# Kernel tuning notes

Measured on AMD Instinct MI355X. Metric: run time of the kernel, lower is better.

The kernel has to match this reference:

```python
import jax, jax.numpy as jnp
import numpy as np

DIM = 1024
NUM_HEADS = 16
HEAD_DIM = DIM // NUM_HEADS


def setup_inputs() -> dict:
    key = jax.random.key(0)
    k1, k2, k3, k4, k5 = jax.random.split(key, 5)
    B, N = 4, 2048
    x = jax.random.normal(k1, (B, N, DIM), dtype=jnp.float32)
    s_in = 1.0 / np.sqrt(DIM)
    W_qkv = jax.random.normal(k2, (DIM, 3 * DIM), dtype=jnp.float32) * s_in
    b_qkv = jax.random.normal(k3, (3 * DIM,), dtype=jnp.float32) * 0.02
    W_proj = jax.random.normal(k4, (DIM, DIM), dtype=jnp.float32) * s_in
    b_proj = jax.random.normal(k5, (DIM,), dtype=jnp.float32) * 0.02
    return {"x": x, "W_qkv": W_qkv, "b_qkv": b_qkv, "W_proj": W_proj, "b_proj": b_proj}


def reference(x, W_qkv, b_qkv, W_proj, b_proj):
    B, N, C = x.shape
    H, D = NUM_HEADS, HEAD_DIM
    scale = D ** -0.5
    qkv = x @ W_qkv + b_qkv                      # [B, N, 3C]
    qkv = qkv.reshape(B, N, 3, H, D)
    q = jnp.transpose(qkv[:, :, 0], (0, 2, 1, 3))  # [B, H, N, D]
    k = jnp.transpose(qkv[:, :, 1], (0, 2, 1, 3))
    v = jnp.transpose(qkv[:, :, 2], (0, 2, 1, 3))
    # scaled dot-product attention (dropout_p=0 in eval)
    attn = jnp.einsum("bhqd,bhkd->bhqk", q, k) * scale
    attn = jax.nn.softmax(attn, axis=-1)
    o = jnp.einsum("bhqk,bhkd->bhqd", attn, v)   # [B, H, N, D]
    o = jnp.transpose(o, (0, 2, 1, 3)).reshape(B, N, C)
    return o @ W_proj + b_proj
```

## Files before the change

### kernel.cpp

```cpp
#include <hip/hip_runtime.h>
#include <cstdint>

#define DIMC 1024
#define NHEAD 16
#define HD 64
#define SEQ 2048
#define NTOK 8192

typedef __attribute__((ext_vector_type(8))) short bfrag;
typedef __attribute__((ext_vector_type(4))) short spack4;
typedef __attribute__((ext_vector_type(4))) float fv4;
typedef __attribute__((ext_vector_type(16))) float f32x16;
typedef __attribute__((ext_vector_type(4))) int iv4;

static __device__ __forceinline__ unsigned short f2bf(float f) {
  union { float f; unsigned int u; } v; v.f = f;
  return (unsigned short)((v.u + 0x7fffu + ((v.u >> 16) & 1u)) >> 16);
}
static __device__ __forceinline__ unsigned int pack2(float a, float b) {
  return (unsigned int)f2bf(a) | ((unsigned int)f2bf(b) << 16);
}

#define MFMA(a, b, c) __builtin_amdgcn_mfma_f32_16x16x32_bf16((a), (b), (c), 0, 0, 0)
#define MFMA32(a, b, c) __builtin_amdgcn_mfma_f32_32x32x16_bf16((a), (b), (c), 0, 0, 0)

__global__ void cvt_x(const float* __restrict__ x, short* __restrict__ xb) {
  int i = (blockIdx.x * 256 + threadIdx.x) * 4;
  fv4 v = *(const fv4*)&x[i];
  spack4 o;
#pragma unroll
  for (int j = 0; j < 4; ++j) o[j] = (short)f2bf(v[j]);
  *(spack4*)&xb[i] = o;
}

__global__ void transpose_w(const float* __restrict__ W, short* __restrict__ WT,
                            int R, int C) {
  __shared__ float tile[32][33];
  const int t = threadIdx.x;
  const int r = t >> 3, c4 = t & 7;
  const int r0 = blockIdx.y * 32, c0 = blockIdx.x * 32;
  fv4 v = *(const fv4*)&W[(size_t)(r0 + r) * C + c0 + c4 * 4];
#pragma unroll
  for (int j = 0; j < 4; ++j) tile[r][c4 * 4 + j] = v[j];
  __syncthreads();
  spack4 o;
#pragma unroll
  for (int j = 0; j < 4; ++j) o[j] = (short)f2bf(tile[c4 * 4 + j][r]);
  *(spack4*)&WT[(size_t)(c0 + r) * R + r0 + c4 * 4] = o;
}

template <int MODE>
__launch_bounds__(256)
__global__ void gemm_bt(const short* __restrict__ A, const short* __restrict__ BT,
                        const float* __restrict__ bias, int M, int N, int K,
                        short* __restrict__ out0, short* __restrict__ out1,
                        short* __restrict__ out2, float* __restrict__ outf) {
  __shared__ alignas(16) char As[128 * 128];
  __shared__ alignas(16) char Bs[128 * 128];
  const int t = threadIdx.x;
  const int lane = t & 63;
  const int wid = t >> 6;
  const int wm = wid >> 1, wn = wid & 1;
  const int g = lane >> 4, l15 = lane & 15;
  const int row0 = blockIdx.y * 128;
  const int col0 = blockIdx.x * 128;
  const int lr = t >> 3, ls = t & 7;

  fv4 acc[4][4] = {};

  for (int k0 = 0; k0 < K; k0 += 64) {
    bfrag av[4], bv[4];
#pragma unroll
    for (int i = 0; i < 4; ++i) {
      int row = lr + i * 32;
      av[i] = *(const bfrag*)&A[(size_t)(row0 + row) * K + k0 + ls * 8];
      bv[i] = *(const bfrag*)&BT[(size_t)(col0 + row) * K + k0 + ls * 8];
    }
    __syncthreads();
#pragma unroll
    for (int i = 0; i < 4; ++i) {
      int row = lr + i * 32;
      int kb = (ls * 16) ^ ((row & 7) << 4);
      *(bfrag*)&As[row * 128 + kb] = av[i];
      *(bfrag*)&Bs[row * 128 + kb] = bv[i];
    }
    __syncthreads();
#pragma unroll
    for (int kk = 0; kk < 2; ++kk) {
      bfrag af[4], bf[4];
#pragma unroll
      for (int mm = 0; mm < 4; ++mm) {
        int row = wm * 64 + mm * 16 + l15;
        af[mm] = *(const bfrag*)&As[row * 128 + ((kk * 64 + g * 16) ^ ((row & 7) << 4))];
      }
#pragma unroll
      for (int nn = 0; nn < 4; ++nn) {
        int row = wn * 64 + nn * 16 + l15;
        bf[nn] = *(const bfrag*)&Bs[row * 128 + ((kk * 64 + g * 16) ^ ((row & 7) << 4))];
      }
#pragma unroll
      for (int mm = 0; mm < 4; ++mm)
#pragma unroll
        for (int nn = 0; nn < 4; ++nn)
          acc[mm][nn] = MFMA(af[mm], bf[nn], acc[mm][nn]);
    }
  }

  if (MODE == 0) {
    const float qs = 0.125f * 1.4426950408889634f;
#pragma unroll
    for (int nn = 0; nn < 4; ++nn) {
      int col = col0 + wn * 64 + nn * 16 + l15;
      int which = col >> 10;
      int rem = col & 1023;
      int h = rem >> 6, d = rem & 63;
      float bval = bias[col];
#pragma unroll
      for (int mm = 0; mm < 4; ++mm) {
        int tok = row0 + wm * 64 + mm * 16 + g * 4;
        int b = tok >> 11, n = tok & 2047;
        int bh = b * NHEAD + h;
        if (which == 0) {
#pragma unroll
          for (int r = 0; r < 4; ++r)
            out0[((size_t)bh * SEQ + n + r) * HD + d] =
                (short)f2bf((acc[mm][nn][r] + bval) * qs);
        } else if (which == 1) {
#pragma unroll
          for (int r = 0; r < 4; ++r)
            out1[((size_t)bh * SEQ + n + r) * HD + d] =
                (short)f2bf(acc[mm][nn][r] + bval);
        } else {
          spack4 p;
#pragma unroll
          for (int r = 0; r < 4; ++r) p[r] = (short)f2bf(acc[mm][nn][r] + bval);
          *(spack4*)&out2[((size_t)bh * HD + d) * SEQ + n] = p;
        }
      }
    }
  } else {
#pragma unroll
    for (int nn = 0; nn < 4; ++nn) {
      int col = col0 + wn * 64 + nn * 16 + l15;
      float bval = bias[col];
#pragma unroll
      for (int mm = 0; mm < 4; ++mm) {
        int tok = row0 + wm * 64 + mm * 16 + g * 4;
#pragma unroll
        for (int r = 0; r < 4; ++r)
          outf[(size_t)(tok + r) * N + col] = acc[mm][nn][r] + bval;
      }
    }
  }
}

__launch_bounds__(256, 3)
__global__ void attn_fwd(const short* __restrict__ Q, const short* __restrict__ Kb,
                         const short* __restrict__ VT, short* __restrict__ O) {
  __shared__ alignas(16) char Ks[2][8192];
  __shared__ alignas(16) char Vs[2][8192];

  const int t = threadIdx.x, lane = t & 63, wid = t >> 6;
  const int l31 = lane & 31, hi = lane >> 5, l7 = lane & 7;

  const int bid = blockIdx.x;
  const int xcd = bid & 7, mm_ = bid >> 3;
  const int bh = xcd + 8 * (mm_ >> 4);
  const int qt = mm_ & 15;

  const size_t base = (size_t)bh * SEQ * HD;
  const short* Qp = Q + base;
  const short* Kp = Kb + base;
  const short* Vp = VT + base;
  const int q0 = qt * 128 + wid * 32;

  bfrag qf[4];
#pragma unroll
  for (int dblk = 0; dblk < 4; ++dblk)
    qf[dblk] = *(const bfrag*)&Qp[(size_t)(q0 + l31) * HD + dblk * 16 + hi * 8];

  f32x16 oacc[2] = {};
  float m = -1e30f, l = 0.f;

  const int sr = t >> 3, ss = t & 7;
  const int swz0 = (ss * 16) ^ ((sr & 7) << 4);

  {
    bfrag k0 = *(const bfrag*)&Kp[(size_t)sr * HD + ss * 8];
    bfrag k1 = *(const bfrag*)&Kp[(size_t)(32 + sr) * HD + ss * 8];
    bfrag v0 = *(const bfrag*)&Vp[(size_t)sr * SEQ + ss * 8];
    bfrag v1 = *(const bfrag*)&Vp[(size_t)(sr + 32) * SEQ + ss * 8];
    *(bfrag*)&Ks[0][sr * 128 + swz0] = k0;
    *(bfrag*)&Ks[0][(sr + 32) * 128 + swz0] = k1;
    *(bfrag*)&Vs[0][sr * 128 + swz0] = v0;
    *(bfrag*)&Vs[0][(sr + 32) * 128 + swz0] = v1;
  }
  __syncthreads();

  int cur = 0;
  for (int kt = 0; kt < SEQ / 64; ++kt) {
    bfrag nk0, nk1, nv0, nv1;
    const bool pre = (kt + 1) < (SEQ / 64);
    if (pre) {
      const int kb2 = (kt + 1) * 64;
      nk0 = *(const bfrag*)&Kp[(size_t)(kb2 + sr) * HD + ss * 8];
      nk1 = *(const bfrag*)&Kp[(size_t)(kb2 + 32 + sr) * HD + ss * 8];
      nv0 = *(const bfrag*)&Vp[(size_t)sr * SEQ + kb2 + ss * 8];
      nv1 = *(const bfrag*)&Vp[(size_t)(sr + 32) * SEQ + kb2 + ss * 8];
    }

    const char* Kc = Ks[cur];
    const char* Vc = Vs[cur];

    f32x16 sf[2] = {};
#pragma unroll
    for (int kb = 0; kb < 2; ++kb) {
#pragma unroll
      for (int dblk = 0; dblk < 4; ++dblk) {
        const int row = kb * 32 + l31;
        bfrag kf = *(const bfrag*)&Kc[row * 128 + ((dblk * 32 + hi * 16) ^ (l7 << 4))];
        sf[kb] = MFMA32(kf, qf[dblk], sf[kb]);
      }
    }

    float pm = sf[0][0];
#pragma unroll
    for (int i = 1; i < 16; ++i) pm = fmaxf(pm, sf[0][i]);
#pragma unroll
    for (int i = 0; i < 16; ++i) pm = fmaxf(pm, sf[1][i]);
    pm = fmaxf(pm, __shfl_xor(pm, 32));

    {
      const float mn = fmaxf(m, pm);
      const float corr = __builtin_amdgcn_exp2f(m - mn);
      m = mn;
      l *= corr;
#pragma unroll
      for (int dh = 0; dh < 2; ++dh)
#pragma unroll
        for (int i = 0; i < 16; ++i) oacc[dh][i] *= corr;
    }

    float sum = 0.f;
#pragma unroll
    for (int kb = 0; kb < 2; ++kb)
#pragma unroll
      for (int i = 0; i < 16; ++i) {
        const float e = __builtin_amdgcn_exp2f(sf[kb][i] - m);
        sf[kb][i] = e;
        sum += e;
      }
    l += sum + __shfl_xor(sum, 32);

#pragma unroll
    for (int hb = 0; hb < 4; ++hb) {
      const int kb = hb >> 1, ob = (hb & 1) * 8;
      const unsigned int x01 = pack2(sf[kb][ob + 0], sf[kb][ob + 1]);
      const unsigned int x23 = pack2(sf[kb][ob + 2], sf[kb][ob + 3]);
      const unsigned int y45 = pack2(sf[kb][ob + 4], sf[kb][ob + 5]);
      const unsigned int y67 = pack2(sf[kb][ob + 6], sf[kb][ob + 7]);
      const unsigned int px01 = (unsigned int)__shfl_xor((int)x01, 32);
      const unsigned int px23 = (unsigned int)__shfl_xor((int)x23, 32);
      const unsigned int py45 = (unsigned int)__shfl_xor((int)y45, 32);
      const unsigned int py67 = (unsigned int)__shfl_xor((int)y67, 32);
      iv4 pw;
      pw[0] = (int)(hi ? py45 : x01);
      pw[1] = (int)(hi ? py67 : x23);
      pw[2] = (int)(hi ? y45 : px01);
      pw[3] = (int)(hi ? y67 : px23);
      const bfrag pb = __builtin_bit_cast(bfrag, pw);
#pragma unroll
      for (int dh = 0; dh < 2; ++dh) {
        const int row = dh * 32 + l31;
        bfrag vf = *(const bfrag*)&Vc[row * 128 + ((hb * 32 + hi * 16) ^ (l7 << 4))];
        oacc[dh] = MFMA32(vf, pb, oacc[dh]);
      }
    }

    if (pre) {
      const int nb = cur ^ 1;
      *(bfrag*)&Ks[nb][sr * 128 + swz0] = nk0;
      *(bfrag*)&Ks[nb][(sr + 32) * 128 + swz0] = nk1;
      *(bfrag*)&Vs[nb][sr * 128 + swz0] = nv0;
      *(bfrag*)&Vs[nb][(sr + 32) * 128 + swz0] = nv1;
      __syncthreads();
    }
    cur ^= 1;
  }

  const float inv = 1.0f / l;
  const int b = bh >> 4, h = bh & 15;
  const int q = q0 + l31;
#pragma unroll
  for (int dh = 0; dh < 2; ++dh)
#pragma unroll
    for (int gp = 0; gp < 4; ++gp) {
      const int d0 = dh * 32 + gp * 8 + hi * 4;
      spack4 pk;
#pragma unroll
      for (int j = 0; j < 4; ++j)
        pk[j] = (short)f2bf(oacc[dh][gp * 4 + j] * inv);
      *(spack4*)&O[((size_t)b * SEQ + q) * DIMC + h * HD + d0] = pk;
    }
}

extern "C" void kernel_launch(void* const* d_in, const int* in_sizes, int n_in,
                              void* d_out, int out_size, void* d_ws, size_t ws_size,
                              hipStream_t stream) {
  const float* x     = (const float*)d_in[0];
  const float* Wqkv  = (const float*)d_in[1];
  const float* bqkv  = (const float*)d_in[2];
  const float* Wproj = (const float*)d_in[3];
  const float* bproj = (const float*)d_in[4];
  float* out = (float*)d_out;
  char* ws = (char*)d_ws;

  short* xb  = (short*)(ws);
  short* WqT = (short*)(ws + 16777216);
  short* WpT = (short*)(ws + 23068672);
  short* Qb  = (short*)(ws + 25165824);
  short* Kb  = (short*)(ws + 41943040);
  short* VTb = (short*)(ws + 58720256);
  short* Ob  = (short*)(ws + 75497472);

  cvt_x<<<8192, 256, 0, stream>>>(x, xb);
  transpose_w<<<dim3(96, 32), 256, 0, stream>>>(Wqkv, WqT, 1024, 3072);
  transpose_w<<<dim3(32, 32), 256, 0, stream>>>(Wproj, WpT, 1024, 1024);
  gemm_bt<0><<<dim3(24, 64), 256, 0, stream>>>(xb, WqT, bqkv, NTOK, 3072, 1024,
                                               Qb, Kb, VTb, nullptr);
  attn_fwd<<<1024, 256, 0, stream>>>(Qb, Kb, VTb, Ob);
  gemm_bt<1><<<dim3(8, 64), 256, 0, stream>>>(Ob, WpT, bproj, NTOK, 1024, 1024,
                                              nullptr, nullptr, nullptr, out);
}
```

Baseline: 228.8 us.

## Use direct global-to-LDS loads in GEMM and drop P-fragment lane shuffles in attention

```diff
diff --git a/kernel.cpp b/kernel.cpp
--- a/kernel.cpp
+++ b/kernel.cpp
@@ -1,4 +1,5 @@
 #include <hip/hip_runtime.h>
+#include <hip/hip_bf16.h>
 #include <cstdint>
 
 #define DIMC 1024
@@ -17,12 +18,21 @@
   union { float f; unsigned int u; } v; v.f = f;
   return (unsigned short)((v.u + 0x7fffu + ((v.u >> 16) & 1u)) >> 16);
 }
-static __device__ __forceinline__ unsigned int pack2(float a, float b) {
-  return (unsigned int)f2bf(a) | ((unsigned int)f2bf(b) << 16);
+static __device__ __forceinline__ unsigned int pack2c(float a, float b) {
+  __hip_bfloat16 ha(a), hb(b);
+  unsigned short ua, ub;
+  __builtin_memcpy(&ua, &ha, 2);
+  __builtin_memcpy(&ub, &hb, 2);
+  return (unsigned int)ua | ((unsigned int)ub << 16);
 }
 
 #define MFMA(a, b, c) __builtin_amdgcn_mfma_f32_16x16x32_bf16((a), (b), (c), 0, 0, 0)
 #define MFMA32(a, b, c) __builtin_amdgcn_mfma_f32_32x32x16_bf16((a), (b), (c), 0, 0, 0)
+
+#define GLOAD_LDS(gp, lp)                                                  \
+  __builtin_amdgcn_global_load_lds(                                        \
+      (const __attribute__((address_space(1))) void*)(gp),                 \
+      (__attribute__((address_space(3))) void*)(lp), 16, 0, 0)
 
 __global__ void cvt_x(const float* __restrict__ x, short* __restrict__ xb) {
   int i = (blockIdx.x * 256 + threadIdx.x) * 4;
@@ -64,25 +74,17 @@
   const int g = lane >> 4, l15 = lane & 15;
   const int row0 = blockIdx.y * 128;
   const int col0 = blockIdx.x * 128;
-  const int lr = t >> 3, ls = t & 7;
 
   fv4 acc[4][4] = {};
 
+  const int srow = t >> 3, sk = (t & 7) * 8;
+
   for (int k0 = 0; k0 < K; k0 += 64) {
-    bfrag av[4], bv[4];
 #pragma unroll
     for (int i = 0; i < 4; ++i) {
-      int row = lr + i * 32;
-      av[i] = *(const bfrag*)&A[(size_t)(row0 + row) * K + k0 + ls * 8];
-      bv[i] = *(const bfrag*)&BT[(size_t)(col0 + row) * K + k0 + ls * 8];
-    }
-    __syncthreads();
-#pragma unroll
-    for (int i = 0; i < 4; ++i) {
-      int row = lr + i * 32;
-      int kb = (ls * 16) ^ ((row & 7) << 4);
-      *(bfrag*)&As[row * 128 + kb] = av[i];
-      *(bfrag*)&Bs[row * 128 + kb] = bv[i];
+      const int row = i * 32 + srow;
+      GLOAD_LDS(&A[(size_t)(row0 + row) * K + k0 + sk], &As[i * 4096 + t * 16]);
+      GLOAD_LDS(&BT[(size_t)(col0 + row) * K + k0 + sk], &Bs[i * 4096 + t * 16]);
     }
     __syncthreads();
 #pragma unroll
@@ -91,12 +93,12 @@
 #pragma unroll
       for (int mm = 0; mm < 4; ++mm) {
         int row = wm * 64 + mm * 16 + l15;
-        af[mm] = *(const bfrag*)&As[row * 128 + ((kk * 64 + g * 16) ^ ((row & 7) << 4))];
+        af[mm] = *(const bfrag*)&As[row * 128 + kk * 64 + g * 16];
       }
 #pragma unroll
       for (int nn = 0; nn < 4; ++nn) {
         int row = wn * 64 + nn * 16 + l15;
-        bf[nn] = *(const bfrag*)&Bs[row * 128 + ((kk * 64 + g * 16) ^ ((row & 7) << 4))];
+        bf[nn] = *(const bfrag*)&Bs[row * 128 + kk * 64 + g * 16];
       }
 #pragma unroll
       for (int mm = 0; mm < 4; ++mm)
@@ -104,6 +106,7 @@
         for (int nn = 0; nn < 4; ++nn)
           acc[mm][nn] = MFMA(af[mm], bf[nn], acc[mm][nn]);
     }
+    __syncthreads();
   }
 
   if (MODE == 0) {
@@ -131,10 +134,11 @@
             out1[((size_t)bh * SEQ + n + r) * HD + d] =
                 (short)f2bf(acc[mm][nn][r] + bval);
         } else {
+          int n2 = (n & ~15) | ((n & 4) << 1) | ((n & 8) >> 1);
           spack4 p;
 #pragma unroll
           for (int r = 0; r < 4; ++r) p[r] = (short)f2bf(acc[mm][nn][r] + bval);
-          *(spack4*)&out2[((size_t)bh * HD + d) * SEQ + n] = p;
+          *(spack4*)&out2[((size_t)bh * HD + d) * SEQ + n2] = p;
         }
       }
     }
@@ -161,7 +165,8 @@
   __shared__ alignas(16) char Vs[2][8192];
 
   const int t = threadIdx.x, lane = t & 63, wid = t >> 6;
-  const int l31 = lane & 31, hi = lane >> 5, l7 = lane & 7;
+  const int l31 = lane & 31, hi = lane >> 5;
+  const int rsw = (l31 & 7) << 4;
 
   const int bid = blockIdx.x;
   const int xcd = bid & 7, mm_ = bid >> 3;
@@ -213,21 +218,24 @@
     const char* Vc = Vs[cur];
 
     f32x16 sf[2] = {};
+    __builtin_amdgcn_s_setprio(1);
 #pragma unroll
     for (int kb = 0; kb < 2; ++kb) {
 #pragma unroll
       for (int dblk = 0; dblk < 4; ++dblk) {
         const int row = kb * 32 + l31;
-        bfrag kf = *(const bfrag*)&Kc[row * 128 + ((dblk * 32 + hi * 16) ^ (l7 << 4))];
+        bfrag kf = *(const bfrag*)&Kc[row * 128 + ((dblk * 32 + hi * 16) ^ rsw)];
         sf[kb] = MFMA32(kf, qf[dblk], sf[kb]);
       }
     }
-
-    float pm = sf[0][0];
-#pragma unroll
-    for (int i = 1; i < 16; ++i) pm = fmaxf(pm, sf[0][i]);
-#pragma unroll
-    for (int i = 0; i < 16; ++i) pm = fmaxf(pm, sf[1][i]);
+    __builtin_amdgcn_s_setprio(0);
+
+    float mx[8];
+#pragma unroll
+    for (int i = 0; i < 8; ++i)
+      mx[i] = fmaxf(fmaxf(sf[0][i], sf[0][i + 8]), fmaxf(sf[1][i], sf[1][i + 8]));
+    float pm = fmaxf(fmaxf(fmaxf(mx[0], mx[1]), fmaxf(mx[2], mx[3])),
+                     fmaxf(fmaxf(mx[4], mx[5]), fmaxf(mx[6], mx[7])));
     pm = fmaxf(pm, __shfl_xor(pm, 32));
 
     {
@@ -241,41 +249,37 @@
         for (int i = 0; i < 16; ++i) oacc[dh][i] *= corr;
     }
 
-    float sum = 0.f;
-#pragma unroll
-    for (int kb = 0; kb < 2; ++kb)
-#pragma unroll
-      for (int i = 0; i < 16; ++i) {
-        const float e = __builtin_amdgcn_exp2f(sf[kb][i] - m);
-        sf[kb][i] = e;
-        sum += e;
-      }
+    float s0 = 0.f, s1 = 0.f, s2 = 0.f, s3 = 0.f;
+#pragma unroll
+    for (int i = 0; i < 8; ++i) {
+      float e0 = __builtin_amdgcn_exp2f(sf[0][i] - m);
+      float e1 = __builtin_amdgcn_exp2f(sf[0][i + 8] - m);
+      float e2 = __builtin_amdgcn_exp2f(sf[1][i] - m);
+      float e3 = __builtin_amdgcn_exp2f(sf[1][i + 8] - m);
+      sf[0][i] = e0; sf[0][i + 8] = e1; sf[1][i] = e2; sf[1][i + 8] = e3;
+      s0 += e0; s1 += e1; s2 += e2; s3 += e3;
+    }
+    float sum = (s0 + s1) + (s2 + s3);
     l += sum + __shfl_xor(sum, 32);
 
+    __builtin_amdgcn_s_setprio(1);
 #pragma unroll
     for (int hb = 0; hb < 4; ++hb) {
       const int kb = hb >> 1, ob = (hb & 1) * 8;
-      const unsigned int x01 = pack2(sf[kb][ob + 0], sf[kb][ob + 1]);
-      const unsigned int x23 = pack2(sf[kb][ob + 2], sf[kb][ob + 3]);
-      const unsigned int y45 = pack2(sf[kb][ob + 4], sf[kb][ob + 5]);
-      const unsigned int y67 = pack2(sf[kb][ob + 6], sf[kb][ob + 7]);
-      const unsigned int px01 = (unsigned int)__shfl_xor((int)x01, 32);
-      const unsigned int px23 = (unsigned int)__shfl_xor((int)x23, 32);
-      const unsigned int py45 = (unsigned int)__shfl_xor((int)y45, 32);
-      const unsigned int py67 = (unsigned int)__shfl_xor((int)y67, 32);
       iv4 pw;
-      pw[0] = (int)(hi ? py45 : x01);
-      pw[1] = (int)(hi ? py67 : x23);
-      pw[2] = (int)(hi ? y45 : px01);
-      pw[3] = (int)(hi ? y67 : px23);
+      pw[0] = (int)pack2c(sf[kb][ob + 0], sf[kb][ob + 1]);
+      pw[1] = (int)pack2c(sf[kb][ob + 2], sf[kb][ob + 3]);
+      pw[2] = (int)pack2c(sf[kb][ob + 4], sf[kb][ob + 5]);
+      pw[3] = (int)pack2c(sf[kb][ob + 6], sf[kb][ob + 7]);
       const bfrag pb = __builtin_bit_cast(bfrag, pw);
 #pragma unroll
       for (int dh = 0; dh < 2; ++dh) {
         const int row = dh * 32 + l31;
-        bfrag vf = *(const bfrag*)&Vc[row * 128 + ((hb * 32 + hi * 16) ^ (l7 << 4))];
+        bfrag vf = *(const bfrag*)&Vc[row * 128 + ((hb * 32 + hi * 16) ^ rsw)];
         oacc[dh] = MFMA32(vf, pb, oacc[dh]);
       }
     }
+    __builtin_amdgcn_s_setprio(0);
 
     if (pre) {
       const int nb = cur ^ 1;
```

New measurement: 232.8 us. About the same (+1.7%).
